# Kernel tuning notes

Hardware: AMD Instinct MI355X
Metric: run time of the kernel (lower is better)

The kernel has to match this reference:

```python
import jax, jax.numpy as jnp
import numpy as np

B, D, H, W, T, C = 2, 16, 16, 16, 16, 96
NH = 4                      # num_heads
WS = (4, 4, 4, 4)           # window size
SS = (2, 2, 2, 2)           # shift size
EPS = 1e-5
HIDDEN = 4 * C


def _compute_mask():
    # Standard Swin shifted-window attention mask, extended to 4D.
    img = np.zeros((D, H, W, T), np.float32)
    sl = [[slice(0, -WS[i]), slice(-WS[i], -SS[i]), slice(-SS[i], None)] for i in range(4)]
    cnt = 0
    for a in sl[0]:
        for b in sl[1]:
            for c in sl[2]:
                for d in sl[3]:
                    img[a, b, c, d] = cnt
                    cnt += 1
    x = img.reshape(D // WS[0], WS[0], H // WS[1], WS[1], W // WS[2], WS[2], T // WS[3], WS[3])
    x = x.transpose(0, 2, 4, 6, 1, 3, 5, 7).reshape(-1, WS[0] * WS[1] * WS[2] * WS[3])
    diff = x[:, None, :] - x[:, :, None]
    return np.where(diff != 0, np.float32(-100.0), np.float32(0.0))


def setup_inputs() -> dict:
    key = jax.random.key(0)
    ks = jax.random.split(key, 6)
    w = lambda k, shape: jax.random.normal(k, shape, jnp.float32) * 0.02
    return {
        'x': jax.random.normal(ks[0], (B, D, H, W, T, C), jnp.float32),
        'mask_matrix': jnp.asarray(_compute_mask()),
        'norm1_g': jnp.ones((C,), jnp.float32), 'norm1_b': jnp.zeros((C,), jnp.float32),
        'qkv_w': w(ks[1], (3 * C, C)), 'qkv_b': jnp.zeros((3 * C,), jnp.float32),
        'proj_w': w(ks[2], (C, C)), 'proj_b': jnp.zeros((C,), jnp.float32),
        'norm2_g': jnp.ones((C,), jnp.float32), 'norm2_b': jnp.zeros((C,), jnp.float32),
        'fc1_w': w(ks[3], (HIDDEN, C)), 'fc1_b': jnp.zeros((HIDDEN,), jnp.float32),
        'fc2_w': w(ks[4], (C, HIDDEN)), 'fc2_b': jnp.zeros((C,), jnp.float32),
    }


def _ln(x, g, b):
    mu = jnp.mean(x, -1, keepdims=True)
    var = jnp.var(x, -1, keepdims=True)
    return (x - mu) * jax.lax.rsqrt(var + EPS) * g + b


def _partition(x):
    # (B, D, H, W, T, C) -> (B*nw, N, C)
    b, c = x.shape[0], x.shape[-1]
    x = x.reshape(b, D // WS[0], WS[0], H // WS[1], WS[1], W // WS[2], WS[2], T // WS[3], WS[3], c)
    x = x.transpose(0, 1, 3, 5, 7, 2, 4, 6, 8, 9)
    return x.reshape(-1, WS[0] * WS[1] * WS[2] * WS[3], c)


def _reverse(win, b):
    c = win.shape[-1]
    x = win.reshape(b, D // WS[0], H // WS[1], W // WS[2], T // WS[3], WS[0], WS[1], WS[2], WS[3], c)
    x = x.transpose(0, 1, 5, 2, 6, 3, 7, 4, 8, 9)
    return x.reshape(b, D, H, W, T, c)


def reference(x, mask_matrix, norm1_g, norm1_b, qkv_w, qkv_b, proj_w, proj_b,
              norm2_g, norm2_b, fc1_w, fc1_b, fc2_w, fc2_b):
    b, c = x.shape[0], x.shape[-1]
    hd = c // NH
    scale = hd ** -0.5
    shortcut = x
    # norm -> (no pad needed: dims divisible by window) -> cyclic shift
    xn = _ln(x, norm1_g, norm1_b)
    xs = jnp.roll(xn, shift=(-SS[0], -SS[1], -SS[2], -SS[3]), axis=(1, 2, 3, 4))
    win = _partition(xs)                              # (B_, N, C)
    B_, N, _ = win.shape
    qkv = (win @ qkv_w.T + qkv_b).reshape(B_, N, 3, NH, hd).transpose(2, 0, 3, 1, 4)
    q, k, v = qkv[0] * scale, qkv[1], qkv[2]          # (B_, NH, N, hd)
    attn = jnp.einsum('bhid,bhjd->bhij', q, k)        # (B_, NH, N, N)
    nw = mask_matrix.shape[0]
    attn = attn.reshape(B_ // nw, nw, NH, N, N) + mask_matrix[None, :, None]
    attn = jax.nn.softmax(attn.reshape(B_, NH, N, N), axis=-1)
    out = jnp.einsum('bhij,bhjd->bhid', attn, v)
    out = out.transpose(0, 2, 1, 3).reshape(B_, N, c)
    out = out @ proj_w.T + proj_b
    xr = _reverse(out, b)
    xr = jnp.roll(xr, shift=SS, axis=(1, 2, 3, 4))    # reverse cyclic shift
    x = shortcut + xr
    # MLP block
    h = _ln(x, norm2_g, norm2_b)
    h = jax.nn.gelu(h @ fc1_w.T + fc1_b, approximate=False)
    return x + (h @ fc2_w.T + fc2_b)
```

## Files before the change

### kernel.cpp

```cpp
#include <hip/hip_runtime.h>

#define TOK   131072
#define BWIN  512

typedef __attribute__((ext_vector_type(8))) short bf16x8;
typedef __attribute__((ext_vector_type(4))) short bf16x4;
typedef __attribute__((ext_vector_type(4))) float f32x4;

__device__ __forceinline__ unsigned short f2us(float f) {
  union { float f; unsigned int i; } x; x.f = f;
  return (unsigned short)((x.i + 0x7fffu + ((x.i >> 16) & 1u)) >> 16);
}
__device__ __forceinline__ unsigned cvtpk(float lo, float hi) {
  unsigned r;
  asm("v_cvt_pk_bf16_f32 %0, %1, %2" : "=v"(r) : "v"(lo), "v"(hi));
  return r;
}
union U8 { uint2 u; bf16x4 v; };

#define IW1   0
#define IW2   36864
#define IQKV  73728
#define IPROJ 104448
#define IMG_SHORTS 116736

__global__ __launch_bounds__(256) void k_prepw(
    const float* __restrict__ fc1_w, const float* __restrict__ fc2_w,
    const float* __restrict__ qkv_w, const float* __restrict__ proj_w,
    unsigned short* __restrict__ img) {
  int i = blockIdx.x * 256 + threadIdx.x;
  const int l = (i >> 3) & 63, j = i & 7;
  const int quad = l >> 4, l15 = l & 15;
  float v = 0.f;
  if (i < 36864) {
    int f = i >> 9; int nc = f / 18, rem = f - nc * 18;
    int ks = rem / 6, nt = rem - ks * 6;
    v = fc1_w[(size_t)(nc * 96 + nt * 16 + l15) * 96 + ks * 32 + quad * 8 + j];
  } else if (i < 73728) {
    int f = (i - 36864) >> 9; int nc = f / 18, rem = f - nc * 18;
    int ks = rem / 6, nt = rem - ks * 6;
    v = fc2_w[(size_t)(nt * 16 + l15) * 384 + nc * 96 + ks * 32 + quad * 8 + j];
  } else if (i < 104448) {
    int f = (i - 73728) >> 9; int h = f / 15, rem = f - h * 15;
    int ks = rem / 5, mt = rem - ks * 5;
    int e = mt * 16 + l15;
    if (e < 72) {
      int grp = e / 24, rr = e - grp * 24;
      v = qkv_w[(size_t)(grp * 96 + h * 24 + rr) * 96 + ks * 32 + quad * 8 + j];
    }
  } else {
    int f = (i - 104448) >> 9; int h = f / 6, nt = f - h * 6;
    int e = quad * 8 + j;
    if (e < 24) v = proj_w[(size_t)(nt * 16 + l15) * 96 + h * 24 + e];
  }
  img[i] = f2us(v);
}

__global__ __launch_bounds__(256) void k_ln1(const float* __restrict__ x,
                                             const float* __restrict__ g,
                                             const float* __restrict__ b,
                                             unsigned short* __restrict__ xn) {
  const int r = threadIdx.x >> 1, hf = threadIdx.x & 1;
  const int t = blockIdx.x * 128 + r;
  const int b_ = t >> 8, n = t & 255;
  const int batch = b_ >> 8, wi = b_ & 255;
  const int wd = (wi >> 6) & 3, wh = (wi >> 4) & 3, ww = (wi >> 2) & 3, wt = wi & 3;
  const int aa = (n >> 6) & 3, bb = (n >> 4) & 3, cc = (n >> 2) & 3, dd = n & 3;
  const int sd = (wd * 4 + aa + 2) & 15, sh = (wh * 4 + bb + 2) & 15;
  const int sw = (ww * 4 + cc + 2) & 15, st = (wt * 4 + dd + 2) & 15;
  const size_t gg = ((((size_t)(batch * 16 + sd) * 16 + sh) * 16 + sw) * 16 + st);

  const float4* base = (const float4*)(x + gg * 96 + hf * 48);
  float v[48];
  float s = 0.f, q2 = 0.f;
  #pragma unroll
  for (int j = 0; j < 12; j++) {
    float4 f = base[j];
    v[4 * j] = f.x; v[4 * j + 1] = f.y; v[4 * j + 2] = f.z; v[4 * j + 3] = f.w;
    s += f.x + f.y + f.z + f.w;
    q2 += f.x * f.x + f.y * f.y + f.z * f.z + f.w * f.w;
  }
  s += __shfl_xor(s, 1); q2 += __shfl_xor(q2, 1);
  const float mu = s * (1.f / 96.f);
  const float var = q2 * (1.f / 96.f) - mu * mu;
  const float rs = rsqrtf(fmaxf(var, 0.f) + 1e-5f);
  unsigned int* row = (unsigned int*)xn + (size_t)t * 48 + hf * 24;
  #pragma unroll
  for (int jj = 0; jj < 24; jj++) {
    int k0 = hf * 48 + 2 * jj;
    float a0 = (v[2 * jj]     - mu) * rs * g[k0]     + b[k0];
    float a1 = (v[2 * jj + 1] - mu) * rs * g[k0 + 1] + b[k0 + 1];
    row[jj] = cvtpk(a0, a1);
  }
}

__global__ __launch_bounds__(256, 2) void k_win(
    const unsigned short* __restrict__ xn, const float* __restrict__ x,
    const unsigned short* __restrict__ img,
    const float* __restrict__ qkv_b, const float* __restrict__ proj_b,
    float* __restrict__ out) {
  __shared__ __align__(16) short s_k[256 * 36];
  __shared__ __align__(16) short s_vt[32 * 260];
  __shared__ __align__(16) short s_scr[4 * 640];
  __shared__ unsigned char s_lb[256];

  const int tid = threadIdx.x;
  const int w = tid >> 6, l = tid & 63, quad = l >> 4, l15 = l & 15;
  const int q0 = w * 64;
  const int b_ = blockIdx.x;
  const int batch = b_ >> 8, wi = b_ & 255;
  const int wd = (wi >> 6) & 3, wh = (wi >> 4) & 3, ww = (wi >> 2) & 3, wt = wi & 3;
  const float scale = 0.20412414523193154f;
  const f32x4 fz = {0.f, 0.f, 0.f, 0.f};

  {
    const int n = tid;
    const int aa = (n >> 6) & 3, bb = (n >> 4) & 3, cc = (n >> 2) & 3, dd = n & 3;
    const int p0 = wd * 4 + aa, p1 = wh * 4 + bb, p2 = ww * 4 + cc, p3 = wt * 4 + dd;
    const int r0 = p0 >= 14 ? 2 : (p0 >= 12 ? 1 : 0);
    const int r1 = p1 >= 14 ? 2 : (p1 >= 12 ? 1 : 0);
    const int r2 = p2 >= 14 ? 2 : (p2 >= 12 ? 1 : 0);
    const int r3 = p3 >= 14 ? 2 : (p3 >= 12 ? 1 : 0);
    s_lb[n] = (unsigned char)(((r0 * 3 + r1) * 3 + r2) * 3 + r3);
    *(uint2*)&s_k[n * 36 + 24] = make_uint2(0u, 0u);
    *(uint2*)&s_k[n * 36 + 28] = make_uint2(0u, 0u);
    unsigned int* vz = (unsigned int*)(s_vt + 24 * 260);
    for (int i = tid; i < 8 * 130; i += 256) vz[i] = 0u;
  }
  __syncthreads();

  unsigned lj4[16];
  #pragma unroll
  for (int km = 0; km < 16; km++)
    lj4[km] = *(const unsigned*)&s_lb[km * 16 + quad * 4];

  f32x4 pacc[4][6];
  #pragma unroll
  for (int mt = 0; mt < 4; mt++)
    #pragma unroll
    for (int nt = 0; nt < 6; nt++) pacc[mt][nt] = fz;

  const unsigned short* xw = xn + (size_t)b_ * 256 * 96;
  const unsigned short* wq = img + IQKV;
  const unsigned short* wp = img + IPROJ;

  for (int h = 0; h < 4; h++) {
    f32x4 acc[5][4];
    #pragma unroll
    for (int mt = 0; mt < 5; mt++)
      #pragma unroll
      for (int nt = 0; nt < 4; nt++) acc[mt][nt] = fz;
    #pragma unroll
    for (int ks = 0; ks < 3; ks++) {
      bf16x8 aw[5];
      #pragma unroll
      for (int mt = 0; mt < 5; mt++)
        aw[mt] = *(const bf16x8*)(wq + ((h * 3 + ks) * 5 + mt) * 512 + l * 8);
      #pragma unroll
      for (int nt = 0; nt < 4; nt++) {
        bf16x8 bx = *(const bf16x8*)(xw + (size_t)(q0 + nt * 16 + l15) * 96 + ks * 32 + quad * 8);
        #pragma unroll
        for (int mt = 0; mt < 5; mt++)
          acc[mt][nt] = __builtin_amdgcn_mfma_f32_16x16x32_bf16(aw[mt], bx, acc[mt][nt], 0, 0, 0);
      }
    }
    U8 qq[2][4];
    #pragma unroll
    for (int mt = 0; mt < 2; mt++) {
      const int e0 = mt * 16 + quad * 4;
      float b0 = qkv_b[h * 24 + e0],     b1 = qkv_b[h * 24 + e0 + 1];
      float b2 = qkv_b[h * 24 + e0 + 2], b3 = qkv_b[h * 24 + e0 + 3];
      #pragma unroll
      for (int nt = 0; nt < 4; nt++) {
        qq[mt][nt].u.x = cvtpk((acc[mt][nt][0] + b0) * scale, (acc[mt][nt][1] + b1) * scale);
        qq[mt][nt].u.y = cvtpk((acc[mt][nt][2] + b2) * scale, (acc[mt][nt][3] + b3) * scale);
      }
    }
    #pragma unroll
    for (int mt = 1; mt < 5; mt++) {
      const int e0 = mt * 16 + quad * 4;
      #pragma unroll
      for (int nt = 0; nt < 4; nt++) {
        const int tok = q0 + nt * 16 + l15;
        if (e0 >= 24 && e0 < 48) {
          const int e = e0 - 24;
          uint2 pk;
          pk.x = cvtpk(acc[mt][nt][0] + qkv_b[96 + h * 24 + e],
                       acc[mt][nt][1] + qkv_b[96 + h * 24 + e + 1]);
          pk.y = cvtpk(acc[mt][nt][2] + qkv_b[96 + h * 24 + e + 2],
                       acc[mt][nt][3] + qkv_b[96 + h * 24 + e + 3]);
          *(uint2*)&s_k[tok * 36 + e] = pk;
        } else if (e0 >= 48 && e0 < 72) {
          const int e = e0 - 48;
          #pragma unroll
          for (int r = 0; r < 4; r++)
            s_vt[(e + r) * 260 + tok] = (short)f2us(acc[mt][nt][r] + qkv_b[192 + h * 24 + e + r]);
        }
      }
    }
    __syncthreads();
    bf16x8 bpw[6];
    #pragma unroll
    for (int nt = 0; nt < 6; nt++)
      bpw[nt] = *(const bf16x8*)(wp + (h * 6 + nt) * 512 + l * 8);
    short* scr = s_scr + w * 640;
    #pragma unroll 1
    for (int mt4 = 0; mt4 < 4; mt4++) {
      const int qt0 = q0 + mt4 * 16;
      f32x4 sc[16];
      #pragma unroll
      for (int km = 0; km < 16; km++) sc[km] = fz;
      const bf16x4 bq0 = qq[0][mt4].v, bq1 = qq[1][mt4].v;
      __builtin_amdgcn_s_setprio(1);
      #pragma unroll
      for (int km = 0; km < 16; km++) {
        bf16x4 ak0 = *(const bf16x4*)&s_k[(km * 16 + l15) * 36 + quad * 4];
        bf16x4 ak1 = *(const bf16x4*)&s_k[(km * 16 + l15) * 36 + 16 + quad * 4];
        sc[km] = __builtin_amdgcn_mfma_f32_16x16x16bf16_1k(ak0, bq0, sc[km], 0, 0, 0);
        sc[km] = __builtin_amdgcn_mfma_f32_16x16x16bf16_1k(ak1, bq1, sc[km], 0, 0, 0);
      }
      __builtin_amdgcn_s_setprio(0);
      const unsigned lq = s_lb[qt0 + l15];
      float rsum = 0.f;
      #pragma unroll
      for (int km = 0; km < 16; km++) {
        unsigned lj = lj4[km];
        float p0 = ((lj & 255u)         == lq) ? __expf(sc[km][0]) : 0.f;
        float p1 = (((lj >> 8) & 255u)  == lq) ? __expf(sc[km][1]) : 0.f;
        float p2 = (((lj >> 16) & 255u) == lq) ? __expf(sc[km][2]) : 0.f;
        float p3 = ((lj >> 24)          == lq) ? __expf(sc[km][3]) : 0.f;
        sc[km][0] = p0; sc[km][1] = p1; sc[km][2] = p2; sc[km][3] = p3;
        rsum += (p0 + p1) + (p2 + p3);
      }
      rsum += __shfl_xor(rsum, 16, 64);
      rsum += __shfl_xor(rsum, 32, 64);
      const float inv = 1.f / rsum;
      f32x4 ov0 = fz, ov1 = fz;
      __builtin_amdgcn_s_setprio(1);
      #pragma unroll
      for (int km = 0; km < 16; km++) {
        U8 bp;
        bp.u.x = cvtpk(sc[km][0], sc[km][1]);
        bp.u.y = cvtpk(sc[km][2], sc[km][3]);
        bf16x4 av0 = *(const bf16x4*)&s_vt[l15 * 260 + km * 16 + quad * 4];
        bf16x4 av1 = *(const bf16x4*)&s_vt[(16 + l15) * 260 + km * 16 + quad * 4];
        ov0 = __builtin_amdgcn_mfma_f32_16x16x16bf16_1k(av0, bp.v, ov0, 0, 0, 0);
        ov1 = __builtin_amdgcn_mfma_f32_16x16x16bf16_1k(av1, bp.v, ov1, 0, 0, 0);
      }
      __builtin_amdgcn_s_setprio(0);
      uint2 o0, o1;
      o0.x = cvtpk(ov0[0] * inv, ov0[1] * inv);
      o0.y = cvtpk(ov0[2] * inv, ov0[3] * inv);
      o1.x = cvtpk(ov1[0] * inv, ov1[1] * inv);
      o1.y = cvtpk(ov1[2] * inv, ov1[3] * inv);
      *(uint2*)&scr[l15 * 40 + quad * 4] = o0;
      *(uint2*)&scr[l15 * 40 + 16 + quad * 4] = o1;
      bf16x8 ao = *(const bf16x8*)&scr[l15 * 40 + quad * 8];
      #pragma unroll
      for (int nt = 0; nt < 6; nt++)
        pacc[mt4][nt] = __builtin_amdgcn_mfma_f32_16x16x32_bf16(ao, bpw[nt], pacc[mt4][nt], 0, 0, 0);
    }
    __syncthreads();
  }

  #pragma unroll
  for (int mt = 0; mt < 4; mt++) {
    #pragma unroll
    for (int r = 0; r < 4; r++) {
      int n = q0 + mt * 16 + quad * 4 + r;
      const int aa = (n >> 6) & 3, bb = (n >> 4) & 3, cc = (n >> 2) & 3, dd = n & 3;
      const int sd = (wd * 4 + aa + 2) & 15, sh = (wh * 4 + bb + 2) & 15;
      const int sw = (ww * 4 + cc + 2) & 15, st = (wt * 4 + dd + 2) & 15;
      const size_t gg = ((((size_t)(batch * 16 + sd) * 16 + sh) * 16 + sw) * 16 + st);
      #pragma unroll
      for (int nt = 0; nt < 6; nt++) {
        int c = nt * 16 + l15;
        out[gg * 96 + c] = x[gg * 96 + c] + proj_b[c] + pacc[mt][nt][r];
      }
    }
  }
}

__global__ __launch_bounds__(256, 3) void k_mlp(
    float* __restrict__ io,
    const float* __restrict__ n2g, const float* __restrict__ n2b,
    const unsigned short* __restrict__ img,
    const float* __restrict__ fc1_b, const float* __restrict__ fc2_b) {
  __shared__ __align__(16) short s_a[128 * 104];
  __shared__ __align__(16) short s_h[128 * 104];

  const int tid = threadIdx.x;
  const int w = tid >> 6, l = tid & 63;
  const int quad = l >> 4, l15 = l & 15;
  const size_t t0 = (size_t)blockIdx.x * 128;
  const f32x4 fz = {0.f, 0.f, 0.f, 0.f};

  {
    const int r = tid >> 1, hf = tid & 1;
    const float4* base = (const float4*)(io + (t0 + r) * 96 + hf * 48);
    float v[48];
    float s = 0.f, q = 0.f;
    #pragma unroll
    for (int j = 0; j < 12; j++) {
      float4 f = base[j];
      v[4 * j] = f.x; v[4 * j + 1] = f.y; v[4 * j + 2] = f.z; v[4 * j + 3] = f.w;
      s += f.x + f.y + f.z + f.w;
      q += f.x * f.x + f.y * f.y + f.z * f.z + f.w * f.w;
    }
    s += __shfl_xor(s, 1); q += __shfl_xor(q, 1);
    const float mu = s * (1.f / 96.f);
    const float var = q * (1.f / 96.f) - mu * mu;
    const float rs = rsqrtf(fmaxf(var, 0.f) + 1e-5f);
    unsigned int* row = (unsigned int*)&s_a[r * 104] + hf * 24;
    #pragma unroll
    for (int jj = 0; jj < 24; jj++) {
      int k0 = hf * 48 + 2 * jj;
      float lo = (v[2 * jj]     - mu) * rs * n2g[k0]     + n2b[k0];
      float hi = (v[2 * jj + 1] - mu) * rs * n2g[k0 + 1] + n2b[k0 + 1];
      row[jj] = cvtpk(lo, hi);
    }
  }

  f32x4 acc2[2][6];
  #pragma unroll
  for (int m = 0; m < 2; m++)
    #pragma unroll
    for (int i = 0; i < 6; i++) acc2[m][i] = fz;

  for (int nc = 0; nc < 4; nc++) {
    f32x4 acc1[2][6];
    #pragma unroll
    for (int m = 0; m < 2; m++)
      #pragma unroll
      for (int i = 0; i < 6; i++) acc1[m][i] = fz;
    #pragma unroll
    for (int ks = 0; ks < 3; ks++) {
      bf16x8 bw[6];
      #pragma unroll
      for (int nt = 0; nt < 6; nt++)
        bw[nt] = *(const bf16x8*)(img + IW1 + ((nc * 3 + ks) * 6 + nt) * 512 + l * 8);
      #pragma unroll
      for (int m = 0; m < 2; m++) {
        bf16x8 af = *(const bf16x8*)&s_a[(w * 32 + m * 16 + l15) * 104 + ks * 32 + quad * 8];
        #pragma unroll
        for (int nt = 0; nt < 6; nt++)
          acc1[m][nt] = __builtin_amdgcn_mfma_f32_16x16x32_bf16(af, bw[nt], acc1[m][nt], 0, 0, 0);
      }
    }
    #pragma unroll
    for (int m = 0; m < 2; m++)
      #pragma unroll
      for (int nt = 0; nt < 6; nt++) {
        int col = nt * 16 + l15;
        float bv = fc1_b[nc * 96 + col];
        #pragma unroll
        for (int r = 0; r < 4; r++) {
          float z = acc1[m][nt][r] + bv;
          float g = 0.5f * z * (1.f + erff(z * 0.70710678118654752f));
          s_h[(w * 32 + m * 16 + quad * 4 + r) * 104 + col] = (short)f2us(g);
        }
      }
    #pragma unroll
    for (int ks = 0; ks < 3; ks++) {
      bf16x8 bw[6];
      #pragma unroll
      for (int nt = 0; nt < 6; nt++)
        bw[nt] = *(const bf16x8*)(img + IW2 + ((nc * 3 + ks) * 6 + nt) * 512 + l * 8);
      #pragma unroll
      for (int m = 0; m < 2; m++) {
        bf16x8 af = *(const bf16x8*)&s_h[(w * 32 + m * 16 + l15) * 104 + ks * 32 + quad * 8];
        #pragma unroll
        for (int nt = 0; nt < 6; nt++)
          acc2[m][nt] = __builtin_amdgcn_mfma_f32_16x16x32_bf16(af, bw[nt], acc2[m][nt], 0, 0, 0);
      }
    }
  }

  #pragma unroll
  for (int m = 0; m < 2; m++)
    #pragma unroll
    for (int nt = 0; nt < 6; nt++) {
      int col = nt * 16 + l15;
      float bv = fc2_b[col];
      #pragma unroll
      for (int r = 0; r < 4; r++) {
        size_t idx = (t0 + w * 32 + m * 16 + quad * 4 + r) * 96 + col;
        io[idx] = io[idx] + acc2[m][nt][r] + bv;
      }
    }
}

extern "C" void kernel_launch(void* const* d_in, const int* in_sizes, int n_in,
                              void* d_out, int out_size, void* d_ws, size_t ws_size,
                              hipStream_t stream) {
  const float* x      = (const float*)d_in[0];
  const float* n1g    = (const float*)d_in[2];
  const float* n1b    = (const float*)d_in[3];
  const float* qkv_w  = (const float*)d_in[4];
  const float* qkv_b  = (const float*)d_in[5];
  const float* proj_w = (const float*)d_in[6];
  const float* proj_b = (const float*)d_in[7];
  const float* n2g    = (const float*)d_in[8];
  const float* n2b    = (const float*)d_in[9];
  const float* fc1_w  = (const float*)d_in[10];
  const float* fc1_b  = (const float*)d_in[11];
  const float* fc2_w  = (const float*)d_in[12];
  const float* fc2_b  = (const float*)d_in[13];
  float* out = (float*)d_out;

  char* ws = (char*)d_ws;
  unsigned short* xn  = (unsigned short*)ws;
  unsigned short* img = (unsigned short*)(ws + 25165824u);

  k_prepw<<<IMG_SHORTS / 256, 256, 0, stream>>>(fc1_w, fc2_w, qkv_w, proj_w, img);
  k_ln1<<<TOK / 128, 256, 0, stream>>>(x, n1g, n1b, xn);
  k_win<<<BWIN, 256, 0, stream>>>(xn, x, img, qkv_b, proj_b, out);
  k_mlp<<<TOK / 128, 256, 0, stream>>>(out, n2g, n2b, img, fc1_b, fc2_b);
}
```

Baseline: 351.6 us.

## Split output projection out of window attention into separate kernel

The per-head projection accumulation (pacc, 96 fp32 registers per lane) and the cached mask labels are removed from the window-attention kernel. Attention outputs are written as bf16 to a global buffer, and a new k_proj kernel does the proj GEMM plus the residual add with the reverse shift. This cuts register pressure so the attention kernel can declare 4 blocks per SM instead of 2. The cost is an extra global round trip of the attention output (131072x96 bf16), one more launch, and mask labels reloaded from LDS inside the softmax loop.

```diff
diff --git a/kernel.cpp b/kernel.cpp
--- a/kernel.cpp
+++ b/kernel.cpp
@@ -22,7 +22,7 @@
 #define IW2   36864
 #define IQKV  73728
 #define IPROJ 104448
-#define IMG_SHORTS 116736
+#define IMG_SHORTS 113664
 
 __global__ __launch_bounds__(256) void k_prepw(
     const float* __restrict__ fc1_w, const float* __restrict__ fc2_w,
@@ -49,9 +49,8 @@
       v = qkv_w[(size_t)(grp * 96 + h * 24 + rr) * 96 + ks * 32 + quad * 8 + j];
     }
   } else {
-    int f = (i - 104448) >> 9; int h = f / 6, nt = f - h * 6;
-    int e = quad * 8 + j;
-    if (e < 24) v = proj_w[(size_t)(nt * 16 + l15) * 96 + h * 24 + e];
+    int f = (i - 104448) >> 9; int ks = f / 6, nt = f - ks * 6;
+    v = proj_w[(size_t)(nt * 16 + l15) * 96 + ks * 32 + quad * 8 + j];
   }
   img[i] = f2us(v);
 }
@@ -94,21 +93,20 @@
   }
 }
 
-__global__ __launch_bounds__(256, 2) void k_win(
-    const unsigned short* __restrict__ xn, const float* __restrict__ x,
+__global__ __launch_bounds__(256, 4) void k_win(
+    const unsigned short* __restrict__ xn,
     const unsigned short* __restrict__ img,
-    const float* __restrict__ qkv_b, const float* __restrict__ proj_b,
-    float* __restrict__ out) {
+    const float* __restrict__ qkv_b,
+    unsigned short* __restrict__ og) {
   __shared__ __align__(16) short s_k[256 * 36];
   __shared__ __align__(16) short s_vt[32 * 260];
-  __shared__ __align__(16) short s_scr[4 * 640];
   __shared__ unsigned char s_lb[256];
 
   const int tid = threadIdx.x;
   const int w = tid >> 6, l = tid & 63, quad = l >> 4, l15 = l & 15;
   const int q0 = w * 64;
   const int b_ = blockIdx.x;
-  const int batch = b_ >> 8, wi = b_ & 255;
+  const int wi = b_ & 255;
   const int wd = (wi >> 6) & 3, wh = (wi >> 4) & 3, ww = (wi >> 2) & 3, wt = wi & 3;
   const float scale = 0.20412414523193154f;
   const f32x4 fz = {0.f, 0.f, 0.f, 0.f};
@@ -129,20 +127,8 @@
   }
   __syncthreads();
 
-  unsigned lj4[16];
-  #pragma unroll
-  for (int km = 0; km < 16; km++)
-    lj4[km] = *(const unsigned*)&s_lb[km * 16 + quad * 4];
-
-  f32x4 pacc[4][6];
-  #pragma unroll
-  for (int mt = 0; mt < 4; mt++)
-    #pragma unroll
-    for (int nt = 0; nt < 6; nt++) pacc[mt][nt] = fz;
-
   const unsigned short* xw = xn + (size_t)b_ * 256 * 96;
   const unsigned short* wq = img + IQKV;
-  const unsigned short* wp = img + IPROJ;
 
   for (int h = 0; h < 4; h++) {
     f32x4 acc[5][4];
@@ -199,11 +185,6 @@
       }
     }
     __syncthreads();
-    bf16x8 bpw[6];
-    #pragma unroll
-    for (int nt = 0; nt < 6; nt++)
-      bpw[nt] = *(const bf16x8*)(wp + (h * 6 + nt) * 512 + l * 8);
-    short* scr = s_scr + w * 640;
     #pragma unroll 1
     for (int mt4 = 0; mt4 < 4; mt4++) {
       const int qt0 = q0 + mt4 * 16;
@@ -224,7 +205,7 @@
       float rsum = 0.f;
       #pragma unroll
       for (int km = 0; km < 16; km++) {
-        unsigned lj = lj4[km];
+        unsigned lj = *(const unsigned*)&s_lb[km * 16 + quad * 4];
         float p0 = ((lj & 255u)         == lq) ? __expf(sc[km][0]) : 0.f;
         float p1 = (((lj >> 8) & 255u)  == lq) ? __expf(sc[km][1]) : 0.f;
         float p2 = (((lj >> 16) & 255u) == lq) ? __expf(sc[km][2]) : 0.f;
@@ -253,21 +234,52 @@
       o0.y = cvtpk(ov0[2] * inv, ov0[3] * inv);
       o1.x = cvtpk(ov1[0] * inv, ov1[1] * inv);
       o1.y = cvtpk(ov1[2] * inv, ov1[3] * inv);
-      *(uint2*)&scr[l15 * 40 + quad * 4] = o0;
-      *(uint2*)&scr[l15 * 40 + 16 + quad * 4] = o1;
-      bf16x8 ao = *(const bf16x8*)&scr[l15 * 40 + quad * 8];
+      size_t ob = ((size_t)b_ * 256 + qt0 + l15) * 96 + h * 24;
+      *(uint2*)&og[ob + quad * 4] = o0;
+      if (quad < 2) *(uint2*)&og[ob + 16 + quad * 4] = o1;
+    }
+    __syncthreads();
+  }
+}
+
+__global__ __launch_bounds__(256, 4) void k_proj(
+    const unsigned short* __restrict__ og, const float* __restrict__ x,
+    const unsigned short* __restrict__ img,
+    const float* __restrict__ proj_b, float* __restrict__ out) {
+  const int tid = threadIdx.x;
+  const int w = tid >> 6, l = tid & 63, quad = l >> 4, l15 = l & 15;
+  const int t0 = blockIdx.x * 128;
+  const f32x4 fz = {0.f, 0.f, 0.f, 0.f};
+
+  f32x4 acc[2][6];
+  #pragma unroll
+  for (int m = 0; m < 2; m++)
+    #pragma unroll
+    for (int nt = 0; nt < 6; nt++) acc[m][nt] = fz;
+
+  #pragma unroll
+  for (int ks = 0; ks < 3; ks++) {
+    bf16x8 bw[6];
+    #pragma unroll
+    for (int nt = 0; nt < 6; nt++)
+      bw[nt] = *(const bf16x8*)(img + IPROJ + (ks * 6 + nt) * 512 + l * 8);
+    #pragma unroll
+    for (int m = 0; m < 2; m++) {
+      bf16x8 af = *(const bf16x8*)(og + (size_t)(t0 + w * 32 + m * 16 + l15) * 96 + ks * 32 + quad * 8);
       #pragma unroll
       for (int nt = 0; nt < 6; nt++)
-        pacc[mt4][nt] = __builtin_amdgcn_mfma_f32_16x16x32_bf16(ao, bpw[nt], pacc[mt4][nt], 0, 0, 0);
-    }
-    __syncthreads();
-  }
-
-  #pragma unroll
-  for (int mt = 0; mt < 4; mt++) {
+        acc[m][nt] = __builtin_amdgcn_mfma_f32_16x16x32_bf16(af, bw[nt], acc[m][nt], 0, 0, 0);
+    }
+  }
+
+  #pragma unroll
+  for (int m = 0; m < 2; m++) {
     #pragma unroll
     for (int r = 0; r < 4; r++) {
-      int n = q0 + mt * 16 + quad * 4 + r;
+      const int T = t0 + w * 32 + m * 16 + quad * 4 + r;
+      const int b_ = T >> 8, n = T & 255;
+      const int batch = b_ >> 8, wi = b_ & 255;
+      const int wd = (wi >> 6) & 3, wh = (wi >> 4) & 3, ww = (wi >> 2) & 3, wt = wi & 3;
       const int aa = (n >> 6) & 3, bb = (n >> 4) & 3, cc = (n >> 2) & 3, dd = n & 3;
       const int sd = (wd * 4 + aa + 2) & 15, sh = (wh * 4 + bb + 2) & 15;
       const int sw = (ww * 4 + cc + 2) & 15, st = (wt * 4 + dd + 2) & 15;
@@ -275,7 +287,7 @@
       #pragma unroll
       for (int nt = 0; nt < 6; nt++) {
         int c = nt * 16 + l15;
-        out[gg * 96 + c] = x[gg * 96 + c] + proj_b[c] + pacc[mt][nt][r];
+        out[gg * 96 + c] = x[gg * 96 + c] + proj_b[c] + acc[m][nt][r];
       }
     }
   }
@@ -411,9 +423,11 @@
   char* ws = (char*)d_ws;
   unsigned short* xn  = (unsigned short*)ws;
   unsigned short* img = (unsigned short*)(ws + 25165824u);
+  unsigned short* og  = (unsigned short*)(ws + 25165824u + 227328u);
 
   k_prepw<<<IMG_SHORTS / 256, 256, 0, stream>>>(fc1_w, fc2_w, qkv_w, proj_w, img);
   k_ln1<<<TOK / 128, 256, 0, stream>>>(x, n1g, n1b, xn);
-  k_win<<<BWIN, 256, 0, stream>>>(xn, x, img, qkv_b, proj_b, out);
+  k_win<<<BWIN, 256, 0, stream>>>(xn, img, qkv_b, og);
+  k_proj<<<TOK / 128, 256, 0, stream>>>(og, x, img, proj_b, out);
   k_mlp<<<TOK / 128, 256, 0, stream>>>(out, n2g, n2b, img, fc1_b, fc2_b);
 }
```

Result: slower. 426.1 us (+21.2%).
